# Kernel tuning notes

Measured on AMD Instinct MI355X. Metric: run time of the kernel, lower is better.

The kernel has to match this reference:

```python
import jax, jax.numpy as jnp
import numpy as np

IN_F, OUT_F, NUM_GRIDS, BATCH = 2048, 2048, 8, 4096


def setup_inputs() -> dict:
    key = jax.random.key(0)
    ks = jax.random.split(key, 5)
    x = jax.random.normal(ks[0], (BATCH, IN_F), dtype=jnp.float32)
    # kaiming_uniform_(a=sqrt(5)) on Linear weight -> U(-b, b), b = 1/sqrt(in_features)
    bound = 1.0 / np.sqrt(IN_F)
    base_w = jax.random.uniform(ks[1], (OUT_F, IN_F), dtype=jnp.float32, minval=-bound, maxval=bound)
    base_b = jnp.zeros((OUT_F,), dtype=jnp.float32)
    spline_weight = 0.1 * jax.random.normal(ks[2], (OUT_F, IN_F, NUM_GRIDS), dtype=jnp.float32)
    grid = jnp.linspace(-2.0, 2.0, NUM_GRIDS, dtype=jnp.float32)
    adaptive_gate = jnp.ones((OUT_F,), dtype=jnp.float32)
    feature_importance = jnp.ones((IN_F,), dtype=jnp.float32)
    return {"x": x, "base_w": base_w, "base_b": base_b,
            "spline_weight": spline_weight, "grid": grid,
            "adaptive_gate": adaptive_gate, "feature_importance": feature_importance}


def reference(x, base_w, base_b, spline_weight, grid, adaptive_gate, feature_importance):
    # feature gating
    x_weighted = x * jax.nn.sigmoid(feature_importance)[None, :]          # [b, i]
    # base path: Linear
    base_output = x_weighted @ base_w.T + base_b                          # [b, o]
    # spline path: RBF basis over grid
    x_norm = jnp.tanh(x_weighted)                                         # [b, i]
    basis = jnp.exp(-((x_norm[:, :, None] - grid[None, None, :]) ** 2) * 2.0)  # [b, i, g]
    # F.normalize(p=1, dim=-1): divide by L1 norm clamped to eps
    denom = jnp.maximum(jnp.sum(jnp.abs(basis), axis=-1, keepdims=True), 1e-12)
    basis = basis / denom
    spline_output = jnp.einsum('big,oig->bo', basis, spline_weight)       # [b, o]
    gate = jax.nn.sigmoid(adaptive_gate)[None, :]                         # [1, o]
    return gate * spline_output + (1.0 - gate) * base_output
```

## Files before the change

### kernel.cpp

```cpp
#include <hip/hip_runtime.h>
#include <hip/hip_bf16.h>

#define IN_F   2048
#define OUT_F  2048
#define NG     8
#define BATCH  4096
#define KDIM   (IN_F * (NG + 1))
#define BK     64
#define NT     (KDIM / BK)
#define BM     256
#define BN     128
#define ASZ    (BM * BK * 2)
#define BSZ    (BN * BK * 2)
#define BUFSZ  (ASZ + BSZ)

typedef short bf16x8 __attribute__((ext_vector_type(8)));
typedef float f32x4  __attribute__((ext_vector_type(4)));
typedef __attribute__((address_space(3))) unsigned char       lds_u8;
typedef const __attribute__((address_space(1))) unsigned char glb_u8;

__device__ __forceinline__ float sigmoidf_(float v) {
    return 1.0f / (1.0f + __expf(-v));
}

__device__ __forceinline__ unsigned short f2bf(float f) {
    unsigned int u = __builtin_bit_cast(unsigned int, f);
    u = (u + 0x7fffu + ((u >> 16) & 1u)) >> 16;
    return (unsigned short)u;
}

__global__ __launch_bounds__(256) void act_kernel(
    const float* __restrict__ x, const float* __restrict__ fi,
    const float* __restrict__ gr, unsigned short* __restrict__ Abf)
{
    const int base = blockIdx.x * 1024;
    const int tid  = threadIdx.x;
    const int b    = base >> 11;
    const float4 g0 = *(const float4*)gr;
    const float4 g1 = *(const float4*)(gr + 4);
    unsigned short* rowp = Abf + (size_t)b * KDIM;

#pragma unroll
    for (int e = 0; e < 4; ++e) {
        const int idx = base + tid + e * 256;
        const int i   = idx & (IN_F - 1);
        const float s  = sigmoidf_(fi[i]);
        const float xw = x[idx] * s;
        const float ex = __expf(2.0f * xw);
        const float xn = (ex - 1.0f) / (ex + 1.0f);

        float ev[NG];
        float d;
        d = xn - g0.x; ev[0] = __expf(-2.0f * d * d);
        d = xn - g0.y; ev[1] = __expf(-2.0f * d * d);
        d = xn - g0.z; ev[2] = __expf(-2.0f * d * d);
        d = xn - g0.w; ev[3] = __expf(-2.0f * d * d);
        d = xn - g1.x; ev[4] = __expf(-2.0f * d * d);
        d = xn - g1.y; ev[5] = __expf(-2.0f * d * d);
        d = xn - g1.z; ev[6] = __expf(-2.0f * d * d);
        d = xn - g1.w; ev[7] = __expf(-2.0f * d * d);
        float denom = ((ev[0] + ev[1]) + (ev[2] + ev[3])) +
                      ((ev[4] + ev[5]) + (ev[6] + ev[7]));
        const float rinv = 1.0f / fmaxf(denom, 1e-12f);

        union { unsigned short us[8]; int4 v; } pk;
#pragma unroll
        for (int g = 0; g < NG; ++g) pk.us[g] = f2bf(ev[g] * rinv);
        *(int4*)(rowp + i * NG) = pk.v;
        rowp[IN_F * NG + i] = f2bf(xw);
    }
}

__global__ __launch_bounds__(256) void wprep_kernel(
    const float* __restrict__ bw, const float* __restrict__ sw,
    const float* __restrict__ ag, unsigned short* __restrict__ Wbf)
{
    const int base = blockIdx.x * 1024;
    const int tid  = threadIdx.x;
    const int o    = base >> 11;
    const float gate = sigmoidf_(ag[o]);
    const float og   = 1.0f - gate;
    unsigned short* rowp = Wbf + (size_t)o * KDIM;

#pragma unroll
    for (int e = 0; e < 4; ++e) {
        const int idx = base + tid + e * 256;
        const int i   = idx & (IN_F - 1);
        const float4 s0 = *(const float4*)(sw + (size_t)idx * NG);
        const float4 s1 = *(const float4*)(sw + (size_t)idx * NG + 4);
        union { unsigned short us[8]; int4 v; } pk;
        pk.us[0] = f2bf(gate * s0.x); pk.us[1] = f2bf(gate * s0.y);
        pk.us[2] = f2bf(gate * s0.z); pk.us[3] = f2bf(gate * s0.w);
        pk.us[4] = f2bf(gate * s1.x); pk.us[5] = f2bf(gate * s1.y);
        pk.us[6] = f2bf(gate * s1.z); pk.us[7] = f2bf(gate * s1.w);
        *(int4*)(rowp + i * NG) = pk.v;
        rowp[IN_F * NG + i] = f2bf(og * bw[idx]);
    }
}

#define MFMA(d, a, b) d = __builtin_amdgcn_mfma_f32_16x16x32_bf16(a, b, d, 0, 0, 0)

#define MFMA8(m0i, m1i, va0, va1)                              \
    __builtin_amdgcn_s_setprio(1);                             \
    MFMA(acc[m0i][0], va0, vb0); MFMA(acc[m0i][1], va0, vb1);  \
    MFMA(acc[m0i][2], va0, vb2); MFMA(acc[m0i][3], va0, vb3);  \
    MFMA(acc[m1i][0], va1, vb0); MFMA(acc[m1i][1], va1, vb1);  \
    MFMA(acc[m1i][2], va1, vb2); MFMA(acc[m1i][3], va1, vb3);  \
    __builtin_amdgcn_s_setprio(0);

#define PHASE_MID()                                            \
    __builtin_amdgcn_sched_barrier(0);                         \
    __builtin_amdgcn_s_barrier();                              \
    asm volatile("s_waitcnt lgkmcnt(0)" ::: "memory");         \
    __builtin_amdgcn_sched_barrier(0);

#define PHASE_END()                                            \
    __builtin_amdgcn_sched_barrier(0);                         \
    __builtin_amdgcn_s_barrier();

#define LDA(kk, m) (*(const bf16x8*)(lds + curBase + (oA##m ^ ((kk) << 6))))
#define LDB(kk, n) (*(const bf16x8*)(lds + curBase + (oB##n ^ ((kk) << 6))))

#define GLA(j) __builtin_amdgcn_global_load_lds((glb_u8*)(aS##j + ko), \
                   (lds_u8*)(lds + stBase + aO##j), 16, 0, 0)
#define GLB(j) __builtin_amdgcn_global_load_lds((glb_u8*)(bS##j + ko), \
                   (lds_u8*)(lds + stBase + bO##j), 16, 0, 0)

__global__ __launch_bounds__(512, 2) void gemm_kernel(
    const unsigned short* __restrict__ A, const unsigned short* __restrict__ B,
    const float* __restrict__ bb, const float* __restrict__ ag,
    float* __restrict__ C)
{
    __shared__ __align__(16) unsigned char lds[3 * BUFSZ];

    const int tid = threadIdx.x;
    const int bid = blockIdx.x;
    const int swz = ((bid & 7) << 5) + (bid >> 3);
    const int bm = swz >> 4, bn = swz & 15;

    const int lane = tid & 63, wid = tid >> 6;
    const int wm = wid >> 1, wn = wid & 1;
    const int fr = lane & 15, kg = lane >> 4;

#define MKSA(j)                                                         \
    const int eA##j = tid + (j) * 512;                                  \
    const int rA_##j = eA##j >> 3, cA_##j = (eA##j & 7) ^ (rA_##j & 7); \
    const unsigned short* aS##j = A + (size_t)(bm * BM + rA_##j) * KDIM + cA_##j * 8; \
    const int aO##j = eA##j * 16;
    MKSA(0) MKSA(1) MKSA(2) MKSA(3)
#define MKSB(j)                                                         \
    const int eB##j = tid + (j) * 512;                                  \
    const int rB_##j = eB##j >> 3, cB_##j = (eB##j & 7) ^ (rB_##j & 7); \
    const unsigned short* bS##j = B + (size_t)(bn * BN + rB_##j) * KDIM + cB_##j * 8; \
    const int bO##j = ASZ + eB##j * 16;
    MKSB(0) MKSB(1)

#define MKOA(m)                                                \
    const int rAm##m = wm * 64 + (m) * 16 + fr;                \
    const int oA##m = rAm##m * 128 + ((kg ^ (rAm##m & 7)) << 4);
    MKOA(0) MKOA(1) MKOA(2) MKOA(3)
#define MKOB(n)                                                \
    const int rBn##n = wn * 64 + (n) * 16 + fr;                \
    const int oB##n = ASZ + rBn##n * 128 + ((kg ^ (rBn##n & 7)) << 4);
    MKOB(0) MKOB(1) MKOB(2) MKOB(3)

    f32x4 acc[4][4] = {};

    {
        const int stBase = 0; const long ko = 0;
        GLA(0); GLA(1); GLA(2); GLA(3); GLB(0); GLB(1);
    }
    {
        const int stBase = BUFSZ; const long ko = BK;
        GLA(0); GLA(1); GLA(2); GLA(3); GLB(0); GLB(1);
    }
    asm volatile("s_waitcnt vmcnt(6)" ::: "memory");
    __builtin_amdgcn_sched_barrier(0);
    __builtin_amdgcn_s_barrier();

    int curBase = 0;
    for (int t = 0; t < NT; ++t) {
        const int stBase = (curBase >= BUFSZ) ? (curBase - BUFSZ)
                                              : (curBase + 2 * BUFSZ);
        const bool doSt = (t + 2) < NT;
        const long ko = (long)(t + 2) * BK;

        bf16x8 vb0 = LDB(0, 0), vb1 = LDB(0, 1), vb2 = LDB(0, 2), vb3 = LDB(0, 3);
        bf16x8 va0 = LDA(0, 0), va1 = LDA(0, 1);
        if (doSt) { GLA(0); GLA(1); }
        PHASE_MID(); MFMA8(0, 1, va0, va1); PHASE_END();

        va0 = LDA(0, 2); va1 = LDA(0, 3);
        if (doSt) { GLA(2); GLA(3); }
        PHASE_MID(); MFMA8(2, 3, va0, va1); PHASE_END();

        vb0 = LDB(1, 0); vb1 = LDB(1, 1); vb2 = LDB(1, 2); vb3 = LDB(1, 3);
        va0 = LDA(1, 0); va1 = LDA(1, 1);
        if (doSt) { GLB(0); GLB(1); }
        PHASE_MID(); MFMA8(0, 1, va0, va1); PHASE_END();

        va0 = LDA(1, 2); va1 = LDA(1, 3);
        PHASE_MID(); MFMA8(2, 3, va0, va1);
        if (t < NT - 2) { asm volatile("s_waitcnt vmcnt(6)" ::: "memory"); }
        else            { asm volatile("s_waitcnt vmcnt(0)" ::: "memory"); }
        PHASE_END();

        curBase = (curBase == 2 * BUFSZ) ? 0 : (curBase + BUFSZ);
    }

    const int colb = bn * BN + wn * 64;
    const int rowb = bm * BM + wm * 64;
#pragma unroll
    for (int n = 0; n < 4; ++n) {
        const int col = colb + n * 16 + fr;
        const float gate = sigmoidf_(ag[col]);
        const float bias = (1.0f - gate) * bb[col];
#pragma unroll
        for (int m = 0; m < 4; ++m) {
            const int r0 = rowb + m * 16 + kg * 4;
#pragma unroll
            for (int j = 0; j < 4; ++j)
                C[(size_t)(r0 + j) * OUT_F + col] = acc[m][n][j] + bias;
        }
    }
}

extern "C" void kernel_launch(void* const* d_in, const int* in_sizes, int n_in,
                              void* d_out, int out_size, void* d_ws, size_t ws_size,
                              hipStream_t stream)
{
    const float* x  = (const float*)d_in[0];
    const float* bw = (const float*)d_in[1];
    const float* bb = (const float*)d_in[2];
    const float* sw = (const float*)d_in[3];
    const float* gr = (const float*)d_in[4];
    const float* ag = (const float*)d_in[5];
    const float* fi = (const float*)d_in[6];
    float* out = (float*)d_out;

    unsigned short* Abf = (unsigned short*)d_ws;
    unsigned short* Wbf = Abf + (size_t)BATCH * KDIM;

    const size_t need = ((size_t)BATCH + OUT_F) * KDIM * sizeof(unsigned short);
    if (ws_size < need) return;

    act_kernel<<<BATCH * IN_F / 1024, 256, 0, stream>>>(x, fi, gr, Abf);
    wprep_kernel<<<OUT_F * IN_F / 1024, 256, 0, stream>>>(bw, sw, ag, Wbf);
    gemm_kernel<<<(BATCH / BM) * (OUT_F / BN), 512, 0, stream>>>(Abf, Wbf, bb, ag, out);
}
```

Measured before the change: 551.1 us.

## Switch GEMM inner loop to 32x32x16 bf16 MFMA with two phases per tile

```diff
diff --git a/kernel.cpp b/kernel.cpp
--- a/kernel.cpp
+++ b/kernel.cpp
@@ -15,7 +15,7 @@
 #define BUFSZ  (ASZ + BSZ)
 
 typedef short bf16x8 __attribute__((ext_vector_type(8)));
-typedef float f32x4  __attribute__((ext_vector_type(4)));
+typedef float f32x16 __attribute__((ext_vector_type(16)));
 typedef __attribute__((address_space(3))) unsigned char       lds_u8;
 typedef const __attribute__((address_space(1))) unsigned char glb_u8;
 
@@ -98,15 +98,7 @@
     }
 }
 
-#define MFMA(d, a, b) d = __builtin_amdgcn_mfma_f32_16x16x32_bf16(a, b, d, 0, 0, 0)
-
-#define MFMA8(m0i, m1i, va0, va1)                              \
-    __builtin_amdgcn_s_setprio(1);                             \
-    MFMA(acc[m0i][0], va0, vb0); MFMA(acc[m0i][1], va0, vb1);  \
-    MFMA(acc[m0i][2], va0, vb2); MFMA(acc[m0i][3], va0, vb3);  \
-    MFMA(acc[m1i][0], va1, vb0); MFMA(acc[m1i][1], va1, vb1);  \
-    MFMA(acc[m1i][2], va1, vb2); MFMA(acc[m1i][3], va1, vb3);  \
-    __builtin_amdgcn_s_setprio(0);
+#define MFMA32(d, a, b) d = __builtin_amdgcn_mfma_f32_32x32x16_bf16(a, b, d, 0, 0, 0)
 
 #define PHASE_MID()                                            \
     __builtin_amdgcn_sched_barrier(0);                         \
@@ -118,8 +110,8 @@
     __builtin_amdgcn_sched_barrier(0);                         \
     __builtin_amdgcn_s_barrier();
 
-#define LDA(kk, m) (*(const bf16x8*)(lds + curBase + (oA##m ^ ((kk) << 6))))
-#define LDB(kk, n) (*(const bf16x8*)(lds + curBase + (oB##n ^ ((kk) << 6))))
+#define LDA(s, m) (*(const bf16x8*)(lds + curBase + (oA##m ^ ((s) << 5))))
+#define LDB(s, n) (*(const bf16x8*)(lds + curBase + (oB##n ^ ((s) << 5))))
 
 #define GLA(j) __builtin_amdgcn_global_load_lds((glb_u8*)(aS##j + ko), \
                    (lds_u8*)(lds + stBase + aO##j), 16, 0, 0)
@@ -140,7 +132,7 @@
 
     const int lane = tid & 63, wid = tid >> 6;
     const int wm = wid >> 1, wn = wid & 1;
-    const int fr = lane & 15, kg = lane >> 4;
+    const int l31 = lane & 31, h = lane >> 5;
 
 #define MKSA(j)                                                         \
     const int eA##j = tid + (j) * 512;                                  \
@@ -156,15 +148,15 @@
     MKSB(0) MKSB(1)
 
 #define MKOA(m)                                                \
-    const int rAm##m = wm * 64 + (m) * 16 + fr;                \
-    const int oA##m = rAm##m * 128 + ((kg ^ (rAm##m & 7)) << 4);
-    MKOA(0) MKOA(1) MKOA(2) MKOA(3)
+    const int rAm##m = wm * 64 + (m) * 32 + l31;               \
+    const int oA##m = rAm##m * 128 + ((h ^ (rAm##m & 7)) << 4);
+    MKOA(0) MKOA(1)
 #define MKOB(n)                                                \
-    const int rBn##n = wn * 64 + (n) * 16 + fr;                \
-    const int oB##n = ASZ + rBn##n * 128 + ((kg ^ (rBn##n & 7)) << 4);
-    MKOB(0) MKOB(1) MKOB(2) MKOB(3)
-
-    f32x4 acc[4][4] = {};
+    const int rBn##n = wn * 64 + (n) * 32 + l31;               \
+    const int oB##n = ASZ + rBn##n * 128 + ((h ^ (rBn##n & 7)) << 4);
+    MKOB(0) MKOB(1)
+
+    f32x16 acc[2][2] = {};
 
     {
         const int stBase = 0; const long ko = 0;
@@ -185,24 +177,34 @@
         const bool doSt = (t + 2) < NT;
         const long ko = (long)(t + 2) * BK;
 
-        bf16x8 vb0 = LDB(0, 0), vb1 = LDB(0, 1), vb2 = LDB(0, 2), vb3 = LDB(0, 3);
-        bf16x8 va0 = LDA(0, 0), va1 = LDA(0, 1);
-        if (doSt) { GLA(0); GLA(1); }
-        PHASE_MID(); MFMA8(0, 1, va0, va1); PHASE_END();
-
-        va0 = LDA(0, 2); va1 = LDA(0, 3);
-        if (doSt) { GLA(2); GLA(3); }
-        PHASE_MID(); MFMA8(2, 3, va0, va1); PHASE_END();
-
-        vb0 = LDB(1, 0); vb1 = LDB(1, 1); vb2 = LDB(1, 2); vb3 = LDB(1, 3);
-        va0 = LDA(1, 0); va1 = LDA(1, 1);
-        if (doSt) { GLB(0); GLB(1); }
-        PHASE_MID(); MFMA8(0, 1, va0, va1); PHASE_END();
-
-        va0 = LDA(1, 2); va1 = LDA(1, 3);
-        PHASE_MID(); MFMA8(2, 3, va0, va1);
-        if (t < NT - 2) { asm volatile("s_waitcnt vmcnt(6)" ::: "memory"); }
-        else            { asm volatile("s_waitcnt vmcnt(0)" ::: "memory"); }
+        bf16x8 a00 = LDA(0, 0), a10 = LDA(0, 1);
+        bf16x8 a01 = LDA(1, 0), a11 = LDA(1, 1);
+        bf16x8 b00 = LDB(0, 0), b10 = LDB(0, 1);
+        bf16x8 b01 = LDB(1, 0), b11 = LDB(1, 1);
+        if (doSt) { GLA(0); GLA(1); GLA(2); }
+        PHASE_MID();
+        __builtin_amdgcn_s_setprio(1);
+        MFMA32(acc[0][0], a00, b00); MFMA32(acc[0][1], a00, b10);
+        MFMA32(acc[1][0], a10, b00); MFMA32(acc[1][1], a10, b10);
+        MFMA32(acc[0][0], a01, b01); MFMA32(acc[0][1], a01, b11);
+        MFMA32(acc[1][0], a11, b01); MFMA32(acc[1][1], a11, b11);
+        __builtin_amdgcn_s_setprio(0);
+        PHASE_END();
+
+        a00 = LDA(2, 0); a10 = LDA(2, 1);
+        a01 = LDA(3, 0); a11 = LDA(3, 1);
+        b00 = LDB(2, 0); b10 = LDB(2, 1);
+        b01 = LDB(3, 0); b11 = LDB(3, 1);
+        if (doSt) { GLA(3); GLB(0); GLB(1); }
+        PHASE_MID();
+        __builtin_amdgcn_s_setprio(1);
+        MFMA32(acc[0][0], a00, b00); MFMA32(acc[0][1], a00, b10);
+        MFMA32(acc[1][0], a10, b00); MFMA32(acc[1][1], a10, b10);
+        MFMA32(acc[0][0], a01, b01); MFMA32(acc[0][1], a01, b11);
+        MFMA32(acc[1][0], a11, b01); MFMA32(acc[1][1], a11, b11);
+        __builtin_amdgcn_s_setprio(0);
+        if (doSt) { asm volatile("s_waitcnt vmcnt(6)" ::: "memory"); }
+        else      { asm volatile("s_waitcnt vmcnt(0)" ::: "memory"); }
         PHASE_END();
 
         curBase = (curBase == 2 * BUFSZ) ? 0 : (curBase + BUFSZ);
@@ -211,16 +213,18 @@
     const int colb = bn * BN + wn * 64;
     const int rowb = bm * BM + wm * 64;
 #pragma unroll
-    for (int n = 0; n < 4; ++n) {
-        const int col = colb + n * 16 + fr;
+    for (int ni = 0; ni < 2; ++ni) {
+        const int col = colb + ni * 32 + l31;
         const float gate = sigmoidf_(ag[col]);
         const float bias = (1.0f - gate) * bb[col];
 #pragma unroll
-        for (int m = 0; m < 4; ++m) {
-            const int r0 = rowb + m * 16 + kg * 4;
-#pragma unroll
-            for (int j = 0; j < 4; ++j)
-                C[(size_t)(r0 + j) * OUT_F + col] = acc[m][n][j] + bias;
+        for (int mi = 0; mi < 2; ++mi) {
+            const int r0 = rowb + mi * 32 + 4 * h;
+#pragma unroll
+            for (int reg = 0; reg < 16; ++reg) {
+                const int row = r0 + (reg & 3) + 8 * (reg >> 2);
+                C[(size_t)row * OUT_F + col] = acc[mi][ni][reg] + bias;
+            }
         }
     }
 }
```

New measurement: 571.4 us. 3.7% more time.
